# Performance work log

Hardware: AMD Instinct MI355X
Metric: run time of the kernel (lower is better)

The kernel has to match this reference:

```python
import jax, jax.numpy as jnp
import numpy as np

B, T, N = 32, 2048, 2048
D, L, TE, H = 512, 256, 1024, 8

def _ln(x, g, b, eps=1e-5):
    m = x.mean(-1, keepdims=True)
    v = ((x - m) ** 2).mean(-1, keepdims=True)
    return (x - m) / jnp.sqrt(v + eps) * g + b

def setup_inputs() -> dict:
    key = jax.random.key(0)
    ks = jax.random.split(key, 12)
    s = 0.02
    return {
        "x": jax.random.normal(ks[0], (B, T, D), jnp.float32),
        "xf": jax.random.normal(ks[1], (B, N, L), jnp.float32),
        "emb": jax.random.normal(ks[2], (B, TE), jnp.float32),
        "norm_g": jnp.ones((D,), jnp.float32),
        "norm_b": jnp.zeros((D,), jnp.float32),
        "tnorm_g": jnp.ones((L,), jnp.float32),
        "tnorm_b": jnp.zeros((L,), jnp.float32),
        "Wq": jax.random.normal(ks[3], (D, D), jnp.float32) * s,
        "bq": jnp.zeros((D,), jnp.float32),
        "Wk": jax.random.normal(ks[4], (L, D), jnp.float32) * s,
        "bk": jnp.zeros((D,), jnp.float32),
        "Wv": jax.random.normal(ks[5], (L, D), jnp.float32) * s,
        "bv": jnp.zeros((D,), jnp.float32),
        "We": jax.random.normal(ks[6], (TE, 2 * D), jnp.float32) * s,
        "be": jnp.zeros((2 * D,), jnp.float32),
        "snorm_g": jnp.ones((D,), jnp.float32),
        "snorm_b": jnp.zeros((D,), jnp.float32),
        "Wo": jax.random.normal(ks[7], (D, D), jnp.float32) * s,
        "bo": jnp.zeros((D,), jnp.float32),
    }

def reference(x, xf, emb, norm_g, norm_b, tnorm_g, tnorm_b, Wq, bq, Wk, bk, Wv, bv,
              We, be, snorm_g, snorm_b, Wo, bo):
    b, t, d = x.shape
    n = xf.shape[1]
    hd = d // H
    # projections with pre-LayerNorms
    q = (_ln(x, norm_g, norm_b) @ Wq + bq).reshape(b, t, H, hd)
    xfn = _ln(xf, tnorm_g, tnorm_b)
    k = (xfn @ Wk + bk).reshape(b, n, H, hd)
    v = (xfn @ Wv + bv).reshape(b, n, H, hd)
    # dual softmax of linear attention: query over head-dim, key over sequence
    q = jax.nn.softmax(q, axis=-1)
    k = jax.nn.softmax(k, axis=1)
    # O(N*d^2) linear attention
    attn = jnp.einsum('bnhd,bnhl->bhdl', k, v)          # [B,H,hd,hd]
    y = jnp.einsum('bthd,bhdl->bthl', q, attn).reshape(b, t, d)
    # StylizationBlock (dropout is identity in eval)
    emb_out = jax.nn.silu(emb) @ We + be                # [B, 2D]
    scale, shift = emb_out[:, None, :d], emb_out[:, None, d:]
    h = _ln(y, snorm_g, snorm_b) * (1.0 + scale) + shift
    h = jax.nn.silu(h) @ Wo + bo
    return x + h
```

## Files before the change

### kernel.cpp

```cpp
#include <hip/hip_runtime.h>
#include <math.h>

#define B_ 32
#define T_ 2048
#define N_ 2048
#define D_ 512
#define L_ 256
#define TE_ 1024
#define H_ 8
#define MROWS 65536
#define KCH 16
#define NC_ 8

typedef __attribute__((ext_vector_type(8))) short short8;
typedef __attribute__((ext_vector_type(4))) float f32x4;

__device__ __forceinline__ unsigned short f2bf(float f) {
  unsigned u = __float_as_uint(f);
  unsigned r = (u + 0x7FFF + ((u >> 16) & 1)) >> 16;
  return (unsigned short)r;
}
__device__ __forceinline__ float bf2f(unsigned short u) {
  return __uint_as_float(((unsigned)u) << 16);
}
__device__ __forceinline__ void gload_lds16(const void* g, void* l) {
  __builtin_amdgcn_global_load_lds(
      (const __attribute__((address_space(1))) void*)g,
      (__attribute__((address_space(3))) void*)l, 16, 0, 0);
}

__device__ __forceinline__ float blockReduceSum(float v, float* ws) {
#pragma unroll
  for (int m = 32; m >= 1; m >>= 1) v += __shfl_xor(v, m, 64);
  int wid = threadIdx.x >> 6;
  int lane = threadIdx.x & 63;
  __syncthreads();
  if (lane == 0) ws[wid] = v;
  __syncthreads();
  return ws[0] + ws[1] + ws[2] + ws[3];
}

template <int COLS>
__global__ void __launch_bounds__(256) ln_rows(const float* __restrict__ in,
                                               const float* __restrict__ g,
                                               const float* __restrict__ bb,
                                               unsigned short* __restrict__ out) {
  constexpr int E = COLS / 256;
  __shared__ float ws[4];
  size_t row = blockIdx.x;
  const float* rp = in + row * COLS;
  float v[E];
  float s = 0.f;
#pragma unroll
  for (int e = 0; e < E; ++e) {
    v[e] = rp[threadIdx.x + e * 256];
    s += v[e];
  }
  s = blockReduceSum(s, ws);
  float mean = s * (1.0f / COLS);
  float q = 0.f;
#pragma unroll
  for (int e = 0; e < E; ++e) {
    float d = v[e] - mean;
    q += d * d;
  }
  q = blockReduceSum(q, ws);
  float rstd = rsqrtf(q * (1.0f / COLS) + 1e-5f);
  unsigned short* op = out + row * COLS;
#pragma unroll
  for (int e = 0; e < E; ++e) {
    int c = threadIdx.x + e * 256;
    op[c] = f2bf((v[e] - mean) * rstd * g[c] + bb[c]);
  }
}

__global__ void __launch_bounds__(256) transcast(const float* __restrict__ W,
                                                 unsigned short* __restrict__ Wt,
                                                 int K, int Ncols) {
  __shared__ float t[32][33];
  int k0 = blockIdx.x * 32, n0 = blockIdx.y * 32;
  int tx = threadIdx.x & 31, ty = threadIdx.x >> 5;
#pragma unroll
  for (int i = 0; i < 32; i += 8)
    t[ty + i][tx] = W[(size_t)(k0 + ty + i) * Ncols + n0 + tx];
  __syncthreads();
#pragma unroll
  for (int i = 0; i < 32; i += 8)
    Wt[(size_t)(n0 + ty + i) * K + k0 + tx] = f2bf(t[tx][ty + i]);
}

template <int KT, bool ADD, bool OUTBF, bool QSM>
__global__ void __launch_bounds__(256) gemm_mfma(const unsigned short* __restrict__ A,
                                                 const unsigned short* __restrict__ Wt,
                                                 const float* __restrict__ bias,
                                                 const float* __restrict__ add,
                                                 void* __restrict__ Cv) {
  __shared__ __align__(16) unsigned short sA[128 * 32];
  __shared__ __align__(16) unsigned short sB[128 * 32];
  int tid = threadIdx.x;
  int w = tid >> 6, lane = tid & 63;
  int quad = lane >> 4, r16 = lane & 15;
  int wr = w >> 1, wc = w & 1;
  size_t m0 = (size_t)blockIdx.y * 128;
  int n0 = blockIdx.x * 128;
  int srow = lane >> 2;
  int scol = (lane & 3) * 8;
  f32x4 acc[4][4] = {};

  for (int k0 = 0; k0 < KT; k0 += 32) {
    __syncthreads();
#pragma unroll
    for (int i = 0; i < 2; ++i) {
      int seg = w * 2 + i;
      gload_lds16(&A[(m0 + seg * 16 + srow) * KT + k0 + scol], &sA[seg * 512]);
    }
#pragma unroll
    for (int i = 0; i < 2; ++i) {
      int seg = w * 2 + i;
      gload_lds16(&Wt[(size_t)(n0 + seg * 16 + srow) * KT + k0 + scol], &sB[seg * 512]);
    }
    __syncthreads();
    short8 af[4], bfr[4];
#pragma unroll
    for (int mi = 0; mi < 4; ++mi)
      af[mi] = *(const short8*)&sA[(wr * 64 + mi * 16 + r16) * 32 + quad * 8];
#pragma unroll
    for (int ni = 0; ni < 4; ++ni)
      bfr[ni] = *(const short8*)&sB[(wc * 64 + ni * 16 + r16) * 32 + quad * 8];
#pragma unroll
    for (int mi = 0; mi < 4; ++mi)
#pragma unroll
      for (int ni = 0; ni < 4; ++ni)
        acc[mi][ni] = __builtin_amdgcn_mfma_f32_16x16x32_bf16(af[mi], bfr[ni], acc[mi][ni], 0, 0, 0);
  }

  float* Cf = (float*)Cv;
  unsigned short* Cb = (unsigned short*)Cv;
#pragma unroll
  for (int mi = 0; mi < 4; ++mi)
#pragma unroll
    for (int r = 0; r < 4; ++r) {
      size_t grow = m0 + wr * 64 + mi * 16 + quad * 4 + r;
      if constexpr (QSM) {
        float v4[4];
        float mx = -1e30f;
#pragma unroll
        for (int ni = 0; ni < 4; ++ni) {
          v4[ni] = acc[mi][ni][r] + bias[n0 + wc * 64 + ni * 16 + r16];
          mx = fmaxf(mx, v4[ni]);
        }
#pragma unroll
        for (int s = 8; s >= 1; s >>= 1) mx = fmaxf(mx, __shfl_xor(mx, s, 64));
        float ssum = 0.f;
#pragma unroll
        for (int ni = 0; ni < 4; ++ni) {
          v4[ni] = expf(v4[ni] - mx);
          ssum += v4[ni];
        }
#pragma unroll
        for (int s = 8; s >= 1; s >>= 1) ssum += __shfl_xor(ssum, s, 64);
        float inv = 1.f / ssum;
#pragma unroll
        for (int ni = 0; ni < 4; ++ni) {
          int gcol = n0 + wc * 64 + ni * 16 + r16;
          Cb[grow * 512 + gcol] = f2bf(v4[ni] * inv);
        }
      } else {
#pragma unroll
        for (int ni = 0; ni < 4; ++ni) {
          int gcol = n0 + wc * 64 + ni * 16 + r16;
          float val = acc[mi][ni][r] + bias[gcol];
          if constexpr (ADD) val += add[grow * 512 + gcol];
          if constexpr (OUTBF)
            Cb[grow * 512 + gcol] = f2bf(val);
          else
            Cf[grow * 512 + gcol] = val;
        }
      }
    }
}

__global__ void __launch_bounds__(256) kstats_part(const float* __restrict__ k,
                                                   float* __restrict__ pmax,
                                                   float* __restrict__ psum) {
  int b = blockIdx.x, cg = blockIdx.y, ch = blockIdx.z;
  int tid = threadIdx.x;
  int lane = tid & 63, slice = tid >> 6;
  int c = cg * 64 + lane;
  constexpr int ROWS = N_ / KCH;
  constexpr int PT = ROWS / 4;
  const float* kp = k + ((size_t)b * N_ + (size_t)ch * ROWS) * D_ + c;
  float v[PT];
#pragma unroll
  for (int i = 0; i < PT; ++i) v[i] = kp[(size_t)(slice + i * 4) * D_];
  float m = v[0];
#pragma unroll
  for (int i = 1; i < PT; ++i) m = fmaxf(m, v[i]);
  float s = 0.f;
#pragma unroll
  for (int i = 0; i < PT; ++i) s += expf(v[i] - m);
  __shared__ float mred[256], sred[256];
  mred[tid] = m;
  sred[tid] = s;
  __syncthreads();
  if (tid < 64) {
    float m0 = mred[tid], m1 = mred[tid + 64], m2 = mred[tid + 128], m3 = mred[tid + 192];
    float mm = fmaxf(fmaxf(m0, m1), fmaxf(m2, m3));
    float ss = sred[tid] * expf(m0 - mm) + sred[tid + 64] * expf(m1 - mm) +
               sred[tid + 128] * expf(m2 - mm) + sred[tid + 192] * expf(m3 - mm);
    pmax[((size_t)b * KCH + ch) * D_ + cg * 64 + tid] = mm;
    psum[((size_t)b * KCH + ch) * D_ + cg * 64 + tid] = ss;
  }
}

__global__ void __launch_bounds__(256) kstats_comb(const float* __restrict__ pmax,
                                                   const float* __restrict__ psum,
                                                   float* __restrict__ kmax,
                                                   float* __restrict__ ksum) {
  int b = blockIdx.x;
  int c = blockIdx.y * 256 + threadIdx.x;
  float pm[KCH];
#pragma unroll
  for (int ch = 0; ch < KCH; ++ch) pm[ch] = pmax[((size_t)b * KCH + ch) * D_ + c];
  float m = pm[0];
#pragma unroll
  for (int ch = 1; ch < KCH; ++ch) m = fmaxf(m, pm[ch]);
  float s = 0.f;
#pragma unroll
  for (int ch = 0; ch < KCH; ++ch)
    s += psum[((size_t)b * KCH + ch) * D_ + c] * expf(pm[ch] - m);
  kmax[b * D_ + c] = m;
  ksum[b * D_ + c] = s;
}

__global__ void __launch_bounds__(256) attn_part_kernel(const float* __restrict__ k,
                                                        const float* __restrict__ v,
                                                        const float* __restrict__ kmax,
                                                        const float* __restrict__ ksum,
                                                        float* __restrict__ part) {
  int b = blockIdx.x, h = blockIdx.y, nc = blockIdx.z;
  int tid = threadIdx.x;
  __shared__ float ks_[32][68];
  __shared__ float vs_[32][68];
  __shared__ float mx[64], is_[64];
  if (tid < 64) {
    mx[tid] = kmax[b * D_ + h * 64 + tid];
    is_[tid] = 1.f / ksum[b * D_ + h * 64 + tid];
  }
  const float* kp = k + ((size_t)b * N_ + nc * 256) * D_ + h * 64;
  const float* vp = v + ((size_t)b * N_ + nc * 256) * D_ + h * 64;
  float acc[4][4] = {};
  int tx = tid & 15, ty = tid >> 4;
  int lr = tid >> 4;
  int c4 = (tid & 15) * 4;
  for (int n0 = 0; n0 < 256; n0 += 32) {
    __syncthreads();
#pragma unroll
    for (int rr = 0; rr < 32; rr += 16) {
      float4 kv = *(const float4*)&kp[(size_t)(n0 + lr + rr) * D_ + c4];
      float4 vv = *(const float4*)&vp[(size_t)(n0 + lr + rr) * D_ + c4];
      ks_[lr + rr][c4 + 0] = expf(kv.x - mx[c4 + 0]) * is_[c4 + 0];
      ks_[lr + rr][c4 + 1] = expf(kv.y - mx[c4 + 1]) * is_[c4 + 1];
      ks_[lr + rr][c4 + 2] = expf(kv.z - mx[c4 + 2]) * is_[c4 + 2];
      ks_[lr + rr][c4 + 3] = expf(kv.w - mx[c4 + 3]) * is_[c4 + 3];
      vs_[lr + rr][c4 + 0] = vv.x;
      vs_[lr + rr][c4 + 1] = vv.y;
      vs_[lr + rr][c4 + 2] = vv.z;
      vs_[lr + rr][c4 + 3] = vv.w;
    }
    __syncthreads();
#pragma unroll
    for (int nn = 0; nn < 32; ++nn) {
      float av[4], bv2[4];
#pragma unroll
      for (int i = 0; i < 4; ++i) av[i] = ks_[nn][ty * 4 + i];
#pragma unroll
      for (int j = 0; j < 4; ++j) bv2[j] = vs_[nn][tx * 4 + j];
#pragma unroll
      for (int i = 0; i < 4; ++i)
#pragma unroll
        for (int j = 0; j < 4; ++j) acc[i][j] += av[i] * bv2[j];
    }
  }
  float* ap = part + ((size_t)(b * H_ + h) * NC_ + nc) * 4096;
#pragma unroll
  for (int i = 0; i < 4; ++i) {
    float4 st = make_float4(acc[i][0], acc[i][1], acc[i][2], acc[i][3]);
    *(float4*)&ap[(ty * 4 + i) * 64 + tx * 4] = st;
  }
}

__global__ void __launch_bounds__(256) attn_reduce(const float* __restrict__ part,
                                                   unsigned short* __restrict__ attnT) {
  size_t o = ((size_t)blockIdx.x * 256 + threadIdx.x) * 4;
  size_t bh = o >> 12;
  size_t e = o & 4095;
  float4 s = make_float4(0.f, 0.f, 0.f, 0.f);
#pragma unroll
  for (int nc = 0; nc < NC_; ++nc) {
    float4 p = *(const float4*)&part[(bh * NC_ + nc) * 4096 + e];
    s.x += p.x;
    s.y += p.y;
    s.z += p.z;
    s.w += p.w;
  }
  int d = (int)(e >> 6);
  int l = (int)(e & 63);
  unsigned short* ab = attnT + bh * 4096;
  ab[(l + 0) * 64 + d] = f2bf(s.x);
  ab[(l + 1) * 64 + d] = f2bf(s.y);
  ab[(l + 2) * 64 + d] = f2bf(s.z);
  ab[(l + 3) * 64 + d] = f2bf(s.w);
}

__global__ void __launch_bounds__(256) embmod(const float* __restrict__ emb,
                                              const float* __restrict__ We,
                                              const float* __restrict__ be,
                                              float* __restrict__ eo) {
  int b = blockIdx.x, tid = threadIdx.x;
  __shared__ float se[TE_];
  for (int i = tid; i < TE_; i += 256) {
    float e = emb[b * TE_ + i];
    se[i] = e / (1.f + expf(-e));
  }
  __syncthreads();
  int j0 = tid * 4;
  float a0 = 0, a1 = 0, a2 = 0, a3 = 0;
  for (int i = 0; i < TE_; ++i) {
    float s = se[i];
    float4 wv = *(const float4*)&We[(size_t)i * 1024 + j0];
    a0 += s * wv.x;
    a1 += s * wv.y;
    a2 += s * wv.z;
    a3 += s * wv.w;
  }
  eo[b * 1024 + j0 + 0] = a0 + be[j0 + 0];
  eo[b * 1024 + j0 + 1] = a1 + be[j0 + 1];
  eo[b * 1024 + j0 + 2] = a2 + be[j0 + 2];
  eo[b * 1024 + j0 + 3] = a3 + be[j0 + 3];
}

__global__ void __launch_bounds__(256) yein_mfma(const unsigned short* __restrict__ qsm,
                                                 const unsigned short* __restrict__ attnT,
                                                 float* __restrict__ y) {
  int b = blockIdx.z, h = blockIdx.y;
  size_t t0 = (size_t)blockIdx.x * 256;
  int tid = threadIdx.x;
  int w = tid >> 6, lane = tid & 63;
  int quad = lane >> 4, r16 = lane & 15;
  int srow = lane >> 2;
  int scol = (lane & 3) * 8;
  __shared__ __align__(16) unsigned short sA[256 * 32];
  __shared__ __align__(16) unsigned short sB[64 * 32];
  const unsigned short* qp = qsm + ((size_t)b * T_ + t0) * D_ + h * 64;
  const unsigned short* bp = attnT + (size_t)(b * H_ + h) * 4096;
  f32x4 acc[4][4] = {};

  for (int k0 = 0; k0 < 64; k0 += 32) {
    __syncthreads();
#pragma unroll
    for (int i = 0; i < 4; ++i) {
      int seg = w * 4 + i;
      gload_lds16(&qp[(size_t)(seg * 16 + srow) * D_ + k0 + scol], &sA[seg * 512]);
    }
    gload_lds16(&bp[(w * 16 + srow) * 64 + k0 + scol], &sB[w * 512]);
    __syncthreads();
    short8 af[4], bfr[4];
#pragma unroll
    for (int mi = 0; mi < 4; ++mi)
      af[mi] = *(const short8*)&sA[(w * 64 + mi * 16 + r16) * 32 + quad * 8];
#pragma unroll
    for (int ni = 0; ni < 4; ++ni)
      bfr[ni] = *(const short8*)&sB[(ni * 16 + r16) * 32 + quad * 8];
#pragma unroll
    for (int mi = 0; mi < 4; ++mi)
#pragma unroll
      for (int ni = 0; ni < 4; ++ni)
        acc[mi][ni] = __builtin_amdgcn_mfma_f32_16x16x32_bf16(af[mi], bfr[ni], acc[mi][ni], 0, 0, 0);
  }

#pragma unroll
  for (int mi = 0; mi < 4; ++mi)
#pragma unroll
    for (int r = 0; r < 4; ++r) {
      size_t grow = t0 + w * 64 + mi * 16 + quad * 4 + r;
      float* yp = y + ((size_t)b * T_ + grow) * D_ + h * 64;
#pragma unroll
      for (int ni = 0; ni < 4; ++ni) yp[ni * 16 + r16] = acc[mi][ni][r];
    }
}

__global__ void __launch_bounds__(256) modln(const float* __restrict__ y,
                                             const float* __restrict__ sg,
                                             const float* __restrict__ sb,
                                             const float* __restrict__ eo,
                                             unsigned short* __restrict__ hs) {
  __shared__ float ws[4];
  size_t row = blockIdx.x;
  int b = (int)(row >> 11);
  const float* rp = y + row * D_;
  float v[2];
  float s = 0.f;
#pragma unroll
  for (int e = 0; e < 2; ++e) {
    v[e] = rp[threadIdx.x + e * 256];
    s += v[e];
  }
  s = blockReduceSum(s, ws);
  float mean = s * (1.0f / D_);
  float q = 0.f;
#pragma unroll
  for (int e = 0; e < 2; ++e) {
    float d = v[e] - mean;
    q += d * d;
  }
  q = blockReduceSum(q, ws);
  float rstd = rsqrtf(q * (1.0f / D_) + 1e-5f);
#pragma unroll
  for (int e = 0; e < 2; ++e) {
    int c = threadIdx.x + e * 256;
    float xm = (v[e] - mean) * rstd * sg[c] + sb[c];
    float sc = eo[b * 1024 + c];
    float sh = eo[b * 1024 + D_ + c];
    float hm = xm * (1.f + sc) + sh;
    hs[row * D_ + c] = f2bf(hm / (1.f + expf(-hm)));
  }
}

extern "C" void kernel_launch(void* const* d_in, const int* in_sizes, int n_in,
                              void* d_out, int out_size, void* d_ws, size_t ws_size,
                              hipStream_t stream) {
  const float* x = (const float*)d_in[0];
  const float* xf = (const float*)d_in[1];
  const float* emb = (const float*)d_in[2];
  const float* norm_g = (const float*)d_in[3];
  const float* norm_b = (const float*)d_in[4];
  const float* tnorm_g = (const float*)d_in[5];
  const float* tnorm_b = (const float*)d_in[6];
  const float* Wq = (const float*)d_in[7];
  const float* bq = (const float*)d_in[8];
  const float* Wk = (const float*)d_in[9];
  const float* bk = (const float*)d_in[10];
  const float* Wv = (const float*)d_in[11];
  const float* bv = (const float*)d_in[12];
  const float* We = (const float*)d_in[13];
  const float* be = (const float*)d_in[14];
  const float* sg = (const float*)d_in[15];
  const float* sb = (const float*)d_in[16];
  const float* Wo = (const float*)d_in[17];
  const float* bo = (const float*)d_in[18];
  float* out = (float*)d_out;

  float* w = (float*)d_ws;
  unsigned short* qbf = (unsigned short*)w;
  float* kbuf = w + 16777216;
  float* vbuf = w + 16777216 + 33554432;
  unsigned short* xnbf = (unsigned short*)(w + 83886080);
  unsigned short* xfnbf = (unsigned short*)(w + 100663296);
  unsigned short* attnT = (unsigned short*)(w + 109051904);
  float* kmaxp = w + 109051904 + 1048576;
  float* ksump = kmaxp + 16384;
  float* embout = ksump + 16384;
  unsigned short* wqt = (unsigned short*)(embout + 32768);
  unsigned short* wkt = wqt + 262144;
  unsigned short* wvt = wkt + 131072;
  unsigned short* wot = wvt + 131072;
  float* pmaxp = w + 83886080;
  float* psump = pmaxp + (size_t)B_ * KCH * D_;
  float* attnpart = w + 100663296;

  transcast<<<dim3(16, 16), 256, 0, stream>>>(Wq, wqt, 512, 512);
  transcast<<<dim3(8, 16), 256, 0, stream>>>(Wk, wkt, 256, 512);
  transcast<<<dim3(8, 16), 256, 0, stream>>>(Wv, wvt, 256, 512);
  transcast<<<dim3(16, 16), 256, 0, stream>>>(Wo, wot, 512, 512);
  ln_rows<512><<<MROWS, 256, 0, stream>>>(x, norm_g, norm_b, xnbf);
  gemm_mfma<512, false, true, true><<<dim3(4, 512), 256, 0, stream>>>(xnbf, wqt, bq, nullptr, qbf);
  ln_rows<256><<<MROWS, 256, 0, stream>>>(xf, tnorm_g, tnorm_b, xfnbf);
  gemm_mfma<256, false, false, false><<<dim3(4, 512), 256, 0, stream>>>(xfnbf, wkt, bk, nullptr, kbuf);
  gemm_mfma<256, false, false, false><<<dim3(4, 512), 256, 0, stream>>>(xfnbf, wvt, bv, nullptr, vbuf);
  kstats_part<<<dim3(32, 8, KCH), 256, 0, stream>>>(kbuf, pmaxp, psump);
  kstats_comb<<<dim3(32, 2), 256, 0, stream>>>(pmaxp, psump, kmaxp, ksump);
  attn_part_kernel<<<dim3(32, 8, NC_), 256, 0, stream>>>(kbuf, vbuf, kmaxp, ksump, attnpart);
  attn_reduce<<<1024, 256, 0, stream>>>(attnpart, attnT);
  embmod<<<32, 256, 0, stream>>>(emb, We, be, embout);
  yein_mfma<<<dim3(8, 8, 32), 256, 0, stream>>>(qbf, attnT, kbuf);
  modln<<<MROWS, 256, 0, stream>>>(kbuf, sg, sb, embout, xnbf);
  gemm_mfma<512, true, false, false><<<dim3(4, 512), 256, 0, stream>>>(xnbf, wot, bo, x, out);
}
```

Baseline: 941.1 us.

## Double-buffer LDS tiles in GEMM, attention reduction, and y-einsum kernels

```diff
diff --git a/kernel.cpp b/kernel.cpp
--- a/kernel.cpp
+++ b/kernel.cpp
@@ -95,8 +95,8 @@
                                                  const float* __restrict__ bias,
                                                  const float* __restrict__ add,
                                                  void* __restrict__ Cv) {
-  __shared__ __align__(16) unsigned short sA[128 * 32];
-  __shared__ __align__(16) unsigned short sB[128 * 32];
+  __shared__ __align__(16) unsigned short sA[2][128 * 32];
+  __shared__ __align__(16) unsigned short sB[2][128 * 32];
   int tid = threadIdx.x;
   int w = tid >> 6, lane = tid & 63;
   int quad = lane >> 4, r16 = lane & 15;
@@ -107,32 +107,44 @@
   int scol = (lane & 3) * 8;
   f32x4 acc[4][4] = {};
 
-  for (int k0 = 0; k0 < KT; k0 += 32) {
+  const unsigned short* Arow0 = &A[(m0 + w * 32 + srow) * KT + scol];
+  const unsigned short* Brow0 = &Wt[(size_t)(n0 + w * 32 + srow) * KT + scol];
+
+#define G_STAGE(buf, k0)                                                          \
+  do {                                                                            \
+    gload_lds16(Arow0 + (k0), &sA[buf][(w * 2 + 0) * 512]);                       \
+    gload_lds16(Arow0 + (size_t)16 * KT + (k0), &sA[buf][(w * 2 + 1) * 512]);     \
+    gload_lds16(Brow0 + (k0), &sB[buf][(w * 2 + 0) * 512]);                       \
+    gload_lds16(Brow0 + (size_t)16 * KT + (k0), &sB[buf][(w * 2 + 1) * 512]);     \
+  } while (0)
+
+#define G_COMPUTE(buf)                                                            \
+  do {                                                                            \
+    short8 af[4], bfr[4];                                                         \
+    _Pragma("unroll") for (int mi = 0; mi < 4; ++mi)                              \
+        af[mi] = *(const short8*)&sA[buf][(wr * 64 + mi * 16 + r16) * 32 + quad * 8]; \
+    _Pragma("unroll") for (int ni = 0; ni < 4; ++ni)                              \
+        bfr[ni] = *(const short8*)&sB[buf][(wc * 64 + ni * 16 + r16) * 32 + quad * 8]; \
+    _Pragma("unroll") for (int mi = 0; mi < 4; ++mi)                              \
+        _Pragma("unroll") for (int ni = 0; ni < 4; ++ni)                          \
+            acc[mi][ni] =                                                         \
+                __builtin_amdgcn_mfma_f32_16x16x32_bf16(af[mi], bfr[ni], acc[mi][ni], 0, 0, 0); \
+  } while (0)
+
+  constexpr int NT = KT / 32;
+  G_STAGE(0, 0);
+  __syncthreads();
+#pragma unroll 1
+  for (int t = 0; t < NT; t += 2) {
+    if (t + 1 < NT) G_STAGE(1, (t + 1) * 32);
+    G_COMPUTE(0);
     __syncthreads();
-#pragma unroll
-    for (int i = 0; i < 2; ++i) {
-      int seg = w * 2 + i;
-      gload_lds16(&A[(m0 + seg * 16 + srow) * KT + k0 + scol], &sA[seg * 512]);
-    }
-#pragma unroll
-    for (int i = 0; i < 2; ++i) {
-      int seg = w * 2 + i;
-      gload_lds16(&Wt[(size_t)(n0 + seg * 16 + srow) * KT + k0 + scol], &sB[seg * 512]);
-    }
+    if (t + 2 < NT) G_STAGE(0, (t + 2) * 32);
+    G_COMPUTE(1);
     __syncthreads();
-    short8 af[4], bfr[4];
-#pragma unroll
-    for (int mi = 0; mi < 4; ++mi)
-      af[mi] = *(const short8*)&sA[(wr * 64 + mi * 16 + r16) * 32 + quad * 8];
-#pragma unroll
-    for (int ni = 0; ni < 4; ++ni)
-      bfr[ni] = *(const short8*)&sB[(wc * 64 + ni * 16 + r16) * 32 + quad * 8];
-#pragma unroll
-    for (int mi = 0; mi < 4; ++mi)
-#pragma unroll
-      for (int ni = 0; ni < 4; ++ni)
-        acc[mi][ni] = __builtin_amdgcn_mfma_f32_16x16x32_bf16(af[mi], bfr[ni], acc[mi][ni], 0, 0, 0);
-  }
+  }
+#undef G_STAGE
+#undef G_COMPUTE
 
   float* Cf = (float*)Cv;
   unsigned short* Cb = (unsigned short*)Cv;
@@ -253,20 +265,34 @@
   int tx = tid & 15, ty = tid >> 4;
   int lr = tid >> 4;
   int c4 = (tid & 15) * 4;
+  float4 kv0, vv0, kv1, vv1;
+  kv0 = *(const float4*)&kp[(size_t)lr * D_ + c4];
+  vv0 = *(const float4*)&vp[(size_t)lr * D_ + c4];
+  kv1 = *(const float4*)&kp[(size_t)(lr + 16) * D_ + c4];
+  vv1 = *(const float4*)&vp[(size_t)(lr + 16) * D_ + c4];
   for (int n0 = 0; n0 < 256; n0 += 32) {
     __syncthreads();
-#pragma unroll
-    for (int rr = 0; rr < 32; rr += 16) {
-      float4 kv = *(const float4*)&kp[(size_t)(n0 + lr + rr) * D_ + c4];
-      float4 vv = *(const float4*)&vp[(size_t)(n0 + lr + rr) * D_ + c4];
-      ks_[lr + rr][c4 + 0] = expf(kv.x - mx[c4 + 0]) * is_[c4 + 0];
-      ks_[lr + rr][c4 + 1] = expf(kv.y - mx[c4 + 1]) * is_[c4 + 1];
-      ks_[lr + rr][c4 + 2] = expf(kv.z - mx[c4 + 2]) * is_[c4 + 2];
-      ks_[lr + rr][c4 + 3] = expf(kv.w - mx[c4 + 3]) * is_[c4 + 3];
-      vs_[lr + rr][c4 + 0] = vv.x;
-      vs_[lr + rr][c4 + 1] = vv.y;
-      vs_[lr + rr][c4 + 2] = vv.z;
-      vs_[lr + rr][c4 + 3] = vv.w;
+    ks_[lr][c4 + 0] = expf(kv0.x - mx[c4 + 0]) * is_[c4 + 0];
+    ks_[lr][c4 + 1] = expf(kv0.y - mx[c4 + 1]) * is_[c4 + 1];
+    ks_[lr][c4 + 2] = expf(kv0.z - mx[c4 + 2]) * is_[c4 + 2];
+    ks_[lr][c4 + 3] = expf(kv0.w - mx[c4 + 3]) * is_[c4 + 3];
+    vs_[lr][c4 + 0] = vv0.x;
+    vs_[lr][c4 + 1] = vv0.y;
+    vs_[lr][c4 + 2] = vv0.z;
+    vs_[lr][c4 + 3] = vv0.w;
+    ks_[lr + 16][c4 + 0] = expf(kv1.x - mx[c4 + 0]) * is_[c4 + 0];
+    ks_[lr + 16][c4 + 1] = expf(kv1.y - mx[c4 + 1]) * is_[c4 + 1];
+    ks_[lr + 16][c4 + 2] = expf(kv1.z - mx[c4 + 2]) * is_[c4 + 2];
+    ks_[lr + 16][c4 + 3] = expf(kv1.w - mx[c4 + 3]) * is_[c4 + 3];
+    vs_[lr + 16][c4 + 0] = vv1.x;
+    vs_[lr + 16][c4 + 1] = vv1.y;
+    vs_[lr + 16][c4 + 2] = vv1.z;
+    vs_[lr + 16][c4 + 3] = vv1.w;
+    if (n0 + 32 < 256) {
+      kv0 = *(const float4*)&kp[(size_t)(n0 + 32 + lr) * D_ + c4];
+      vv0 = *(const float4*)&vp[(size_t)(n0 + 32 + lr) * D_ + c4];
+      kv1 = *(const float4*)&kp[(size_t)(n0 + 48 + lr) * D_ + c4];
+      vv1 = *(const float4*)&vp[(size_t)(n0 + 48 + lr) * D_ + c4];
     }
     __syncthreads();
 #pragma unroll
@@ -350,28 +376,32 @@
   int quad = lane >> 4, r16 = lane & 15;
   int srow = lane >> 2;
   int scol = (lane & 3) * 8;
-  __shared__ __align__(16) unsigned short sA[256 * 32];
-  __shared__ __align__(16) unsigned short sB[64 * 32];
+  __shared__ __align__(16) unsigned short sA[2][256 * 32];
+  __shared__ __align__(16) unsigned short sB[2][64 * 32];
   const unsigned short* qp = qsm + ((size_t)b * T_ + t0) * D_ + h * 64;
   const unsigned short* bp = attnT + (size_t)(b * H_ + h) * 4096;
   f32x4 acc[4][4] = {};
 
-  for (int k0 = 0; k0 < 64; k0 += 32) {
-    __syncthreads();
+#pragma unroll
+  for (int half = 0; half < 2; ++half) {
+    int k0 = half * 32;
 #pragma unroll
     for (int i = 0; i < 4; ++i) {
       int seg = w * 4 + i;
-      gload_lds16(&qp[(size_t)(seg * 16 + srow) * D_ + k0 + scol], &sA[seg * 512]);
+      gload_lds16(&qp[(size_t)(seg * 16 + srow) * D_ + k0 + scol], &sA[half][seg * 512]);
     }
-    gload_lds16(&bp[(w * 16 + srow) * 64 + k0 + scol], &sB[w * 512]);
-    __syncthreads();
+    gload_lds16(&bp[(w * 16 + srow) * 64 + k0 + scol], &sB[half][w * 512]);
+  }
+  __syncthreads();
+#pragma unroll
+  for (int half = 0; half < 2; ++half) {
     short8 af[4], bfr[4];
 #pragma unroll
     for (int mi = 0; mi < 4; ++mi)
-      af[mi] = *(const short8*)&sA[(w * 64 + mi * 16 + r16) * 32 + quad * 8];
+      af[mi] = *(const short8*)&sA[half][(w * 64 + mi * 16 + r16) * 32 + quad * 8];
 #pragma unroll
     for (int ni = 0; ni < 4; ++ni)
-      bfr[ni] = *(const short8*)&sB[(ni * 16 + r16) * 32 + quad * 8];
+      bfr[ni] = *(const short8*)&sB[half][(ni * 16 + r16) * 32 + quad * 8];
 #pragma unroll
     for (int mi = 0; mi < 4; ++mi)
 #pragma unroll
```

New measurement: 926.3 us. No clear change (-1.6%).
